# Kernel optimization log

Measured on AMD Instinct MI355X. Metric: run time of the kernel, lower is better.

The kernel has to match this reference:

```python
import jax, jax.numpy as jnp
import numpy as np

N = 50000
E = 800000
EPS = 1e-16
NEG_SLOPE = 0.2

def setup_inputs() -> dict:
    key = jax.random.key(0)
    ks = jax.random.split(key, 10)
    s = lambda fan: 1.0 / np.sqrt(fan)
    return {
        "x": jax.random.normal(ks[0], (N, 128), dtype=jnp.float32),
        "edge_index": jax.random.randint(ks[1], (2, E), 0, N, dtype=jnp.int64),
        "W1": jax.random.normal(ks[2], (128, 4 * 32), dtype=jnp.float32) * s(128),
        "att_src1": jax.random.normal(ks[3], (4, 32), dtype=jnp.float32) * s(32),
        "att_dst1": jax.random.normal(ks[4], (4, 32), dtype=jnp.float32) * s(32),
        "b1": jnp.zeros((128,), dtype=jnp.float32),
        "W2": jax.random.normal(ks[5], (128, 2), dtype=jnp.float32) * s(128),
        "att_src2": jax.random.normal(ks[6], (1, 2), dtype=jnp.float32) * s(2),
        "att_dst2": jax.random.normal(ks[7], (1, 2), dtype=jnp.float32) * s(2),
        "b2": jnp.zeros((2,), dtype=jnp.float32),
    }

def _gat_conv(x, src, dst, W, att_src, att_dst, bias, heads, out_ch, concat):
    n = x.shape[0]
    h = (x @ W).reshape(n, heads, out_ch)                      # [N,H,C]
    a_src = jnp.sum(h * att_src[None], axis=-1)                # [N,H]
    a_dst = jnp.sum(h * att_dst[None], axis=-1)                # [N,H]
    e = jax.nn.leaky_relu(a_src[src] + a_dst[dst], NEG_SLOPE)  # [Etot,H]
    # segment softmax over incoming edges per destination node
    m = jax.ops.segment_max(e, dst, num_segments=n)            # [N,H]
    m = jnp.where(jnp.isfinite(m), m, 0.0)
    ex = jnp.exp(e - m[dst])
    denom = jax.ops.segment_sum(ex, dst, num_segments=n)       # [N,H]
    alpha = ex / (denom[dst] + EPS)                            # [Etot,H]
    out = jax.ops.segment_sum(alpha[:, :, None] * h[src], dst, num_segments=n)  # [N,H,C]
    if concat:
        out = out.reshape(n, heads * out_ch)
    else:
        out = out.mean(axis=1)
    return out + bias

def reference(x, edge_index, W1, att_src1, att_dst1, b1, W2, att_src2, att_dst2, b2):
    n = x.shape[0]
    # PyG GATConv adds self-loops by default
    loops = jnp.arange(n, dtype=edge_index.dtype)
    src = jnp.concatenate([edge_index[0], loops])
    dst = jnp.concatenate([edge_index[1], loops])
    # dropout is identity at inference
    h = jax.nn.elu(_gat_conv(x, src, dst, W1, att_src1, att_dst1, b1, 4, 32, True))
    h = _gat_conv(h, src, dst, W2, att_src2, att_dst2, b2, 1, 2, False)
    return jax.nn.log_softmax(h, axis=1)
```

## Files before the change

kernel.cpp:

```cpp
#include <hip/hip_runtime.h>
#include <hip/hip_bf16.h>

#define NN 50000
#define EE 800000
#define ET (EE + NN)
#define CAP 64
#define NEG_SLOPE 0.2f
#define EPSF 1e-16f
#define BUILD_BLOCKS 4096
#define GEMM_BLOCKS ((NN + 63) / 64)

typedef unsigned int uint32;
typedef __attribute__((ext_vector_type(8))) short short8;
typedef __attribute__((ext_vector_type(4))) float floatx4;

__device__ __forceinline__ unsigned short f2bf(float f) {
  unsigned int u = __float_as_uint(f);
  unsigned int r = (u + 0x7fffu + ((u >> 16) & 1u)) >> 16;
  return (unsigned short)r;
}
__device__ __forceinline__ float bf_lo(uint32 v) { return __uint_as_float(v << 16); }
__device__ __forceinline__ float bf_hi(uint32 v) { return __uint_as_float(v & 0xffff0000u); }


__device__ __forceinline__ void do_build(int b, int nb, const int* __restrict__ ei,
                                         int* __restrict__ counts,
                                         int* __restrict__ csr) {
  const int range = b & 7;
  const int lo = range * (NN / 8);
  const int hi = lo + (NN / 8);
  const int group = b >> 3;
  const int ngr = nb >> 3;
  for (int i = group * 256 + threadIdx.x; i < ET; i += ngr * 256) {
    int d = (i < EE) ? ei[EE + i] : (i - EE);
    if (d >= lo && d < hi) {
      int s = (i < EE) ? ei[i] : d;
      int r = atomicAdd(&counts[d], 1);
      if (r < CAP) csr[d * CAP + r] = s;
    }
  }
}

__device__ __forceinline__ void do_gemm_tile(
    int tile, const float* __restrict__ x, const unsigned short* __restrict__ Wt,
    const float* __restrict__ att_src1, const float* __restrict__ att_dst1,
    uint32* __restrict__ h1b, float* __restrict__ as1, float* __restrict__ ad1) {
  const int t    = threadIdx.x;
  const int wave = t >> 6;
  const int lane = t & 63;
  const int quad = lane >> 4;
  const int col  = lane & 15;
  const int nodeBase = tile * 64 + wave * 16;

  floatx4 acc[8];
  #pragma unroll
  for (int i = 0; i < 8; i++) acc[i] = (floatx4){0.f, 0.f, 0.f, 0.f};

  int mread = nodeBase + col; if (mread >= NN) mread = NN - 1;
  const float* __restrict__ xrow = x + (size_t)mread * 128 + quad * 8;
  const unsigned short* __restrict__ bbase = Wt + col * 128 + quad * 8;

  #pragma unroll
  for (int ks = 0; ks < 4; ks++) {
    float4 a0 = *(const float4*)(xrow + ks * 32);
    float4 a1 = *(const float4*)(xrow + ks * 32 + 4);
    union { short8 v; unsigned short u[8]; } af;
    af.u[0] = f2bf(a0.x); af.u[1] = f2bf(a0.y);
    af.u[2] = f2bf(a0.z); af.u[3] = f2bf(a0.w);
    af.u[4] = f2bf(a1.x); af.u[5] = f2bf(a1.y);
    af.u[6] = f2bf(a1.z); af.u[7] = f2bf(a1.w);
    #pragma unroll
    for (int tt = 0; tt < 8; tt++) {
      short8 bf = *(const short8*)(bbase + tt * 16 * 128 + ks * 32);
      acc[tt] = __builtin_amdgcn_mfma_f32_16x16x32_bf16(af.v, bf, acc[tt], 0, 0, 0);
    }
  }

  float asv[8], adv[8];
  #pragma unroll
  for (int tt = 0; tt < 8; tt++) {
    asv[tt] = att_src1[tt * 16 + col];
    adv[tt] = att_dst1[tt * 16 + col];
  }

  #pragma unroll
  for (int r = 0; r < 4; r++) {
    const int gn = nodeBase + quad * 4 + r;
    const bool live = (gn < NN);
    #pragma unroll
    for (int tt = 0; tt < 8; tt++) {
      float v = acc[tt][r];
      float w = __shfl_xor(v, 1, 64);
      if (live && ((col & 1) == 0)) {
        uint32 pk = (uint32)f2bf(v) | ((uint32)f2bf(w) << 16);
        h1b[(size_t)gn * 64 + tt * 8 + (col >> 1)] = pk;
      }
    }
    #pragma unroll
    for (int h = 0; h < 4; h++) {
      float ps = acc[2 * h][r] * asv[2 * h] + acc[2 * h + 1][r] * asv[2 * h + 1];
      float pd = acc[2 * h][r] * adv[2 * h] + acc[2 * h + 1][r] * adv[2 * h + 1];
      #pragma unroll
      for (int off = 1; off < 16; off <<= 1) {
        ps += __shfl_xor(ps, off, 64);
        pd += __shfl_xor(pd, off, 64);
      }
      if (live && col == 0) {
        as1[gn * 4 + h] = ps;
        ad1[gn * 4 + h] = pd;
      }
    }
  }
}

__device__ __forceinline__ void do_agg1_group(
    int g, const int* __restrict__ counts, const int* __restrict__ csr,
    const uint32* __restrict__ h1b, const float* __restrict__ as1,
    const float* __restrict__ ad1, const float* __restrict__ b1,
    const float* __restrict__ W2, const float* __restrict__ att_src2,
    const float* __restrict__ att_dst2,
    float* __restrict__ h2, float* __restrict__ as2, float* __restrict__ ad2) {
  const int lane = threadIdx.x & 63;
  const int wv = threadIdx.x >> 6;
  const int hd = lane >> 4;
  const int n = __builtin_amdgcn_readfirstlane(g * 4 + wv);

  const int cnt = __builtin_amdgcn_readfirstlane(counts[n]);
  const int* __restrict__ row = csr + n * CAP;
  const float adv = ad1[n * 4 + hd];

  float den = 0.f, accx = 0.f, accy = 0.f;
  int j = 0;
  for (; j + 3 < cnt; j += 4) {
    int s0 = row[j], s1 = row[j + 1], s2 = row[j + 2], s3 = row[j + 3];
    float e0 = as1[s0 * 4 + hd] + adv;
    float e1 = as1[s1 * 4 + hd] + adv;
    float e2 = as1[s2 * 4 + hd] + adv;
    float e3 = as1[s3 * 4 + hd] + adv;
    uint32 v0 = h1b[s0 * 64 + lane];
    uint32 v1 = h1b[s1 * 64 + lane];
    uint32 v2 = h1b[s2 * 64 + lane];
    uint32 v3 = h1b[s3 * 64 + lane];
    e0 = (e0 > 0.f) ? e0 : NEG_SLOPE * e0;
    e1 = (e1 > 0.f) ? e1 : NEG_SLOPE * e1;
    e2 = (e2 > 0.f) ? e2 : NEG_SLOPE * e2;
    e3 = (e3 > 0.f) ? e3 : NEG_SLOPE * e3;
    float x0 = __expf(e0), x1 = __expf(e1), x2 = __expf(e2), x3 = __expf(e3);
    den += (x0 + x1) + (x2 + x3);
    accx = fmaf(x0, bf_lo(v0), accx);
    accy = fmaf(x0, bf_hi(v0), accy);
    accx = fmaf(x1, bf_lo(v1), accx);
    accy = fmaf(x1, bf_hi(v1), accy);
    accx = fmaf(x2, bf_lo(v2), accx);
    accy = fmaf(x2, bf_hi(v2), accy);
    accx = fmaf(x3, bf_lo(v3), accx);
    accy = fmaf(x3, bf_hi(v3), accy);
  }
  for (; j < cnt; j++) {
    int s = row[j];
    float e = as1[s * 4 + hd] + adv;
    e = (e > 0.f) ? e : NEG_SLOPE * e;
    float ex = __expf(e);
    uint32 v = h1b[s * 64 + lane];
    den += ex;
    accx = fmaf(ex, bf_lo(v), accx);
    accy = fmaf(ex, bf_hi(v), accy);
  }

  float inv = 1.f / (den + EPSF);
  float2 bb = ((const float2*)b1)[lane];
  float ox = accx * inv + bb.x;
  float oy = accy * inv + bb.y;
  ox = (ox > 0.f) ? ox : (__expf(ox) - 1.f);
  oy = (oy > 0.f) ? oy : (__expf(oy) - 1.f);

  float4 wq = ((const float4*)W2)[lane];
  float p0 = ox * wq.x + oy * wq.z;
  float p1 = ox * wq.y + oy * wq.w;
  #pragma unroll
  for (int off = 32; off; off >>= 1) {
    p0 += __shfl_xor(p0, off, 64);
    p1 += __shfl_xor(p1, off, 64);
  }
  if (lane == 0) {
    *(float2*)&h2[n * 2] = make_float2(p0, p1);
    as2[n] = p0 * att_src2[0] + p1 * att_src2[1];
    ad2[n] = p0 * att_dst2[0] + p1 * att_dst2[1];
  }
}

__device__ __forceinline__ void do_agg2_item(
    int i, const int* __restrict__ counts, const int* __restrict__ csr,
    const float* __restrict__ h2, const float* __restrict__ as2,
    const float* __restrict__ ad2, const float* __restrict__ b2,
    float* __restrict__ out) {
  int n = i >> 3;
  int sub = i & 7;
  const float adv = ad2[n];
  const int cnt = counts[n];
  const int* __restrict__ row = csr + n * CAP;
  const float2* __restrict__ h2v = (const float2*)h2;

  float den = 0.f, a0 = 0.f, a1 = 0.f;
  for (int j = sub; j < cnt; j += 8) {
    int s = row[j];
    float e = as2[s] + adv;
    e = (e > 0.f) ? e : NEG_SLOPE * e;
    float ex = __expf(e);
    float2 hv = h2v[s];
    den += ex;
    a0 = fmaf(ex, hv.x, a0);
    a1 = fmaf(ex, hv.y, a1);
  }
  #pragma unroll
  for (int off = 4; off; off >>= 1) {
    den += __shfl_down(den, off, 8);
    a0  += __shfl_down(a0, off, 8);
    a1  += __shfl_down(a1, off, 8);
  }
  if (sub == 0) {
    float inv = 1.f / (den + EPSF);
    float o0 = a0 * inv + b2[0];
    float o1 = a1 * inv + b2[1];
    float mx = fmaxf(o0, o1);
    float lse = mx + __logf(__expf(o0 - mx) + __expf(o1 - mx));
    *(float2*)&out[n * 2] = make_float2(o0 - lse, o1 - lse);
  }
}

__global__ __launch_bounds__(256) void prep_zero_k(
    const float* __restrict__ W1, unsigned short* __restrict__ Wt,
    int* __restrict__ counts) {
  const int step = gridDim.x * 256;
  for (int i = blockIdx.x * 256 + threadIdx.x; i < NN; i += step) counts[i] = 0;
  for (int i = blockIdx.x * 256 + threadIdx.x; i < 128 * 128; i += step) {
    int k = i >> 7, c = i & 127;
    Wt[c * 128 + k] = f2bf(W1[i]);
  }
}

__global__ __launch_bounds__(256) void work_k(
    const int* __restrict__ ei, int* __restrict__ counts, int* __restrict__ csr,
    const float* __restrict__ x, const unsigned short* __restrict__ Wt,
    const float* __restrict__ att_src1, const float* __restrict__ att_dst1,
    uint32* __restrict__ h1b, float* __restrict__ as1, float* __restrict__ ad1) {
  const int b = blockIdx.x;
  if (b < BUILD_BLOCKS) {
    do_build(b, BUILD_BLOCKS, ei, counts, csr);
  } else {
    do_gemm_tile(b - BUILD_BLOCKS, x, Wt, att_src1, att_dst1, h1b, as1, ad1);
  }
}

__global__ __launch_bounds__(256) void agg1_k(
    const int* __restrict__ counts, const int* __restrict__ csr,
    const uint32* __restrict__ h1b, const float* __restrict__ as1,
    const float* __restrict__ ad1, const float* __restrict__ b1,
    const float* __restrict__ W2, const float* __restrict__ att_src2,
    const float* __restrict__ att_dst2,
    float* __restrict__ h2, float* __restrict__ as2, float* __restrict__ ad2) {
  do_agg1_group(blockIdx.x, counts, csr, h1b, as1, ad1, b1, W2,
                att_src2, att_dst2, h2, as2, ad2);
}

__global__ __launch_bounds__(256) void agg2_k(
    const int* __restrict__ counts, const int* __restrict__ csr,
    const float* __restrict__ h2, const float* __restrict__ as2,
    const float* __restrict__ ad2, const float* __restrict__ b2,
    float* __restrict__ out) {
  int i = blockIdx.x * 256 + threadIdx.x;
  if (i < NN * 8) do_agg2_item(i, counts, csr, h2, as2, ad2, b2, out);
}

extern "C" void kernel_launch(void* const* d_in, const int* in_sizes, int n_in,
                              void* d_out, int out_size, void* d_ws, size_t ws_size,
                              hipStream_t stream) {
  const float* x        = (const float*)d_in[0];
  const int*   ei       = (const int*)d_in[1];
  const float* W1       = (const float*)d_in[2];
  const float* att_src1 = (const float*)d_in[3];
  const float* att_dst1 = (const float*)d_in[4];
  const float* b1       = (const float*)d_in[5];
  const float* W2       = (const float*)d_in[6];
  const float* att_src2 = (const float*)d_in[7];
  const float* att_dst2 = (const float*)d_in[8];
  const float* b2       = (const float*)d_in[9];
  float* out = (float*)d_out;

  char* p = (char*)d_ws;
  auto alloc = [&](size_t bytes) {
    char* r = p;
    p += (bytes + 255) & ~size_t(255);
    return r;
  };
  uint32* h1b  = (uint32*)alloc(sizeof(uint32) * NN * 64);
  float* as1   = (float*)alloc(sizeof(float) * NN * 4);
  float* ad1   = (float*)alloc(sizeof(float) * NN * 4);
  float* h2    = (float*)alloc(sizeof(float) * NN * 2);
  float* as2   = (float*)alloc(sizeof(float) * NN);
  float* ad2   = (float*)alloc(sizeof(float) * NN);
  int*   counts = (int*)alloc(sizeof(int) * NN);
  int*   csr   = (int*)alloc(sizeof(int) * NN * CAP);
  unsigned short* Wt = (unsigned short*)alloc(sizeof(unsigned short) * 128 * 128);

  prep_zero_k<<<256, 256, 0, stream>>>(W1, Wt, counts);
  work_k<<<BUILD_BLOCKS + GEMM_BLOCKS, 256, 0, stream>>>(
      ei, counts, csr, x, Wt, att_src1, att_dst1, h1b, as1, ad1);
  agg1_k<<<NN / 4, 256, 0, stream>>>(counts, csr, h1b, as1, ad1, b1, W2,
                                     att_src2, att_dst2, h2, as2, ad2);
  agg2_k<<<(NN * 8 + 255) / 256, 256, 0, stream>>>(counts, csr, h2, as2, ad2,
                                                   b2, out);
}
```

Measured before the change: 195.8 us.

## Store CSR as 16-bit indices, vectorize edge loads, handle self-loops inline

CSR neighbor indices are now stored as 16-bit values, which fit because the node count is below 65536. This halves the scattered CSR write and read traffic. The build loop reads edge endpoints as int4 vectors and no longer inserts self-loops into the CSR. Instead, both aggregation kernels add the self-loop term directly from the node's own features, and agg1 fetches four neighbor indices with a single 8-byte load. This relies on the node count staying under 65536, and the self-loop no longer uses up a slot in the capped rows.

```diff
diff --git a/kernel.cpp b/kernel.cpp
--- a/kernel.cpp
+++ b/kernel.cpp
@@ -3,7 +3,6 @@
 
 #define NN 50000
 #define EE 800000
-#define ET (EE + NN)
 #define CAP 64
 #define NEG_SLOPE 0.2f
 #define EPSF 1e-16f
@@ -11,6 +10,7 @@
 #define GEMM_BLOCKS ((NN + 63) / 64)
 
 typedef unsigned int uint32;
+typedef unsigned short ushort16;
 typedef __attribute__((ext_vector_type(8))) short short8;
 typedef __attribute__((ext_vector_type(4))) float floatx4;
 
@@ -21,22 +21,36 @@
 }
 __device__ __forceinline__ float bf_lo(uint32 v) { return __uint_as_float(v << 16); }
 __device__ __forceinline__ float bf_hi(uint32 v) { return __uint_as_float(v & 0xffff0000u); }
-
+__device__ __forceinline__ float lrelu(float e) { return (e > 0.f) ? e : NEG_SLOPE * e; }
 
 __device__ __forceinline__ void do_build(int b, int nb, const int* __restrict__ ei,
                                          int* __restrict__ counts,
-                                         int* __restrict__ csr) {
+                                         ushort16* __restrict__ csr) {
   const int range = b & 7;
   const int lo = range * (NN / 8);
   const int hi = lo + (NN / 8);
   const int group = b >> 3;
   const int ngr = nb >> 3;
-  for (int i = group * 256 + threadIdx.x; i < ET; i += ngr * 256) {
-    int d = (i < EE) ? ei[EE + i] : (i - EE);
-    if (d >= lo && d < hi) {
-      int s = (i < EE) ? ei[i] : d;
-      int r = atomicAdd(&counts[d], 1);
-      if (r < CAP) csr[d * CAP + r] = s;
+  const int4* __restrict__ dst4 = (const int4*)(ei + EE);
+  const int4* __restrict__ src4 = (const int4*)ei;
+  for (int c = group * 256 + threadIdx.x; c < EE / 4; c += ngr * 256) {
+    int4 d = dst4[c];
+    int4 s = src4[c];
+    if (d.x >= lo && d.x < hi) {
+      int r = atomicAdd(&counts[d.x], 1);
+      if (r < CAP) csr[d.x * CAP + r] = (ushort16)s.x;
+    }
+    if (d.y >= lo && d.y < hi) {
+      int r = atomicAdd(&counts[d.y], 1);
+      if (r < CAP) csr[d.y * CAP + r] = (ushort16)s.y;
+    }
+    if (d.z >= lo && d.z < hi) {
+      int r = atomicAdd(&counts[d.z], 1);
+      if (r < CAP) csr[d.z * CAP + r] = (ushort16)s.z;
+    }
+    if (d.w >= lo && d.w < hi) {
+      int r = atomicAdd(&counts[d.w], 1);
+      if (r < CAP) csr[d.w * CAP + r] = (ushort16)s.w;
     }
   }
 }
@@ -113,26 +127,56 @@
   }
 }
 
-__device__ __forceinline__ void do_agg1_group(
-    int g, const int* __restrict__ counts, const int* __restrict__ csr,
+__global__ __launch_bounds__(256) void prep_zero_k(
+    const float* __restrict__ W1, unsigned short* __restrict__ Wt,
+    int* __restrict__ counts) {
+  const int step = gridDim.x * 256;
+  for (int i = blockIdx.x * 256 + threadIdx.x; i < NN; i += step) counts[i] = 0;
+  for (int i = blockIdx.x * 256 + threadIdx.x; i < 128 * 128; i += step) {
+    int k = i >> 7, c = i & 127;
+    Wt[c * 128 + k] = f2bf(W1[i]);
+  }
+}
+
+__global__ __launch_bounds__(256) void work_k(
+    const int* __restrict__ ei, int* __restrict__ counts, ushort16* __restrict__ csr,
+    const float* __restrict__ x, const unsigned short* __restrict__ Wt,
+    const float* __restrict__ att_src1, const float* __restrict__ att_dst1,
+    uint32* __restrict__ h1b, float* __restrict__ as1, float* __restrict__ ad1) {
+  const int b = blockIdx.x;
+  if (b < BUILD_BLOCKS) {
+    do_build(b, BUILD_BLOCKS, ei, counts, csr);
+  } else {
+    do_gemm_tile(b - BUILD_BLOCKS, x, Wt, att_src1, att_dst1, h1b, as1, ad1);
+  }
+}
+
+__global__ __launch_bounds__(256) void agg1_k(
+    const int* __restrict__ counts, const ushort16* __restrict__ csr,
     const uint32* __restrict__ h1b, const float* __restrict__ as1,
     const float* __restrict__ ad1, const float* __restrict__ b1,
     const float* __restrict__ W2, const float* __restrict__ att_src2,
     const float* __restrict__ att_dst2,
     float* __restrict__ h2, float* __restrict__ as2, float* __restrict__ ad2) {
   const int lane = threadIdx.x & 63;
-  const int wv = threadIdx.x >> 6;
+  const int n = __builtin_amdgcn_readfirstlane(blockIdx.x * 4 + (threadIdx.x >> 6));
   const int hd = lane >> 4;
-  const int n = __builtin_amdgcn_readfirstlane(g * 4 + wv);
 
   const int cnt = __builtin_amdgcn_readfirstlane(counts[n]);
-  const int* __restrict__ row = csr + n * CAP;
+  const ushort16* __restrict__ row = csr + n * CAP;
   const float adv = ad1[n * 4 + hd];
 
-  float den = 0.f, accx = 0.f, accy = 0.f;
+  float es = lrelu(as1[n * 4 + hd] + adv);
+  float xs = __expf(es);
+  uint32 vs = h1b[n * 64 + lane];
+  float den = xs;
+  float accx = xs * bf_lo(vs), accy = xs * bf_hi(vs);
+
   int j = 0;
   for (; j + 3 < cnt; j += 4) {
-    int s0 = row[j], s1 = row[j + 1], s2 = row[j + 2], s3 = row[j + 3];
+    union { uint2 v; ushort16 u[4]; } ss;
+    ss.v = *(const uint2*)(row + j);
+    int s0 = ss.u[0], s1 = ss.u[1], s2 = ss.u[2], s3 = ss.u[3];
     float e0 = as1[s0 * 4 + hd] + adv;
     float e1 = as1[s1 * 4 + hd] + adv;
     float e2 = as1[s2 * 4 + hd] + adv;
@@ -141,11 +185,8 @@
     uint32 v1 = h1b[s1 * 64 + lane];
     uint32 v2 = h1b[s2 * 64 + lane];
     uint32 v3 = h1b[s3 * 64 + lane];
-    e0 = (e0 > 0.f) ? e0 : NEG_SLOPE * e0;
-    e1 = (e1 > 0.f) ? e1 : NEG_SLOPE * e1;
-    e2 = (e2 > 0.f) ? e2 : NEG_SLOPE * e2;
-    e3 = (e3 > 0.f) ? e3 : NEG_SLOPE * e3;
-    float x0 = __expf(e0), x1 = __expf(e1), x2 = __expf(e2), x3 = __expf(e3);
+    float x0 = __expf(lrelu(e0)), x1 = __expf(lrelu(e1));
+    float x2 = __expf(lrelu(e2)), x3 = __expf(lrelu(e3));
     den += (x0 + x1) + (x2 + x3);
     accx = fmaf(x0, bf_lo(v0), accx);
     accy = fmaf(x0, bf_hi(v0), accy);
@@ -158,8 +199,7 @@
   }
   for (; j < cnt; j++) {
     int s = row[j];
-    float e = as1[s * 4 + hd] + adv;
-    e = (e > 0.f) ? e : NEG_SLOPE * e;
+    float e = lrelu(as1[s * 4 + hd] + adv);
     float ex = __expf(e);
     uint32 v = h1b[s * 64 + lane];
     den += ex;
@@ -189,24 +229,29 @@
   }
 }
 
-__device__ __forceinline__ void do_agg2_item(
-    int i, const int* __restrict__ counts, const int* __restrict__ csr,
+__global__ __launch_bounds__(256) void agg2_k(
+    const int* __restrict__ counts, const ushort16* __restrict__ csr,
     const float* __restrict__ h2, const float* __restrict__ as2,
     const float* __restrict__ ad2, const float* __restrict__ b2,
     float* __restrict__ out) {
+  int i = blockIdx.x * 256 + threadIdx.x;
+  if (i >= NN * 8) return;
   int n = i >> 3;
   int sub = i & 7;
   const float adv = ad2[n];
   const int cnt = counts[n];
-  const int* __restrict__ row = csr + n * CAP;
+  const ushort16* __restrict__ row = csr + n * CAP;
   const float2* __restrict__ h2v = (const float2*)h2;
 
   float den = 0.f, a0 = 0.f, a1 = 0.f;
+  if (sub == 0) {
+    float xs = __expf(lrelu(as2[n] + adv));
+    float2 hv = h2v[n];
+    den = xs; a0 = xs * hv.x; a1 = xs * hv.y;
+  }
   for (int j = sub; j < cnt; j += 8) {
     int s = row[j];
-    float e = as2[s] + adv;
-    e = (e > 0.f) ? e : NEG_SLOPE * e;
-    float ex = __expf(e);
+    float ex = __expf(lrelu(as2[s] + adv));
     float2 hv = h2v[s];
     den += ex;
     a0 = fmaf(ex, hv.x, a0);
@@ -226,50 +271,6 @@
     float lse = mx + __logf(__expf(o0 - mx) + __expf(o1 - mx));
     *(float2*)&out[n * 2] = make_float2(o0 - lse, o1 - lse);
   }
-}
-
-__global__ __launch_bounds__(256) void prep_zero_k(
-    const float* __restrict__ W1, unsigned short* __restrict__ Wt,
-    int* __restrict__ counts) {
-  const int step = gridDim.x * 256;
-  for (int i = blockIdx.x * 256 + threadIdx.x; i < NN; i += step) counts[i] = 0;
-  for (int i = blockIdx.x * 256 + threadIdx.x; i < 128 * 128; i += step) {
-    int k = i >> 7, c = i & 127;
-    Wt[c * 128 + k] = f2bf(W1[i]);
-  }
-}
-
-__global__ __launch_bounds__(256) void work_k(
-    const int* __restrict__ ei, int* __restrict__ counts, int* __restrict__ csr,
-    const float* __restrict__ x, const unsigned short* __restrict__ Wt,
-    const float* __restrict__ att_src1, const float* __restrict__ att_dst1,
-    uint32* __restrict__ h1b, float* __restrict__ as1, float* __restrict__ ad1) {
-  const int b = blockIdx.x;
-  if (b < BUILD_BLOCKS) {
-    do_build(b, BUILD_BLOCKS, ei, counts, csr);
-  } else {
-    do_gemm_tile(b - BUILD_BLOCKS, x, Wt, att_src1, att_dst1, h1b, as1, ad1);
-  }
-}
-
-__global__ __launch_bounds__(256) void agg1_k(
-    const int* __restrict__ counts, const int* __restrict__ csr,
-    const uint32* __restrict__ h1b, const float* __restrict__ as1,
-    const float* __restrict__ ad1, const float* __restrict__ b1,
-    const float* __restrict__ W2, const float* __restrict__ att_src2,
-    const float* __restrict__ att_dst2,
-    float* __restrict__ h2, float* __restrict__ as2, float* __restrict__ ad2) {
-  do_agg1_group(blockIdx.x, counts, csr, h1b, as1, ad1, b1, W2,
-                att_src2, att_dst2, h2, as2, ad2);
-}
-
-__global__ __launch_bounds__(256) void agg2_k(
-    const int* __restrict__ counts, const int* __restrict__ csr,
-    const float* __restrict__ h2, const float* __restrict__ as2,
-    const float* __restrict__ ad2, const float* __restrict__ b2,
-    float* __restrict__ out) {
-  int i = blockIdx.x * 256 + threadIdx.x;
-  if (i < NN * 8) do_agg2_item(i, counts, csr, h2, as2, ad2, b2, out);
 }
 
 extern "C" void kernel_launch(void* const* d_in, const int* in_sizes, int n_in,
@@ -300,7 +301,7 @@
   float* as2   = (float*)alloc(sizeof(float) * NN);
   float* ad2   = (float*)alloc(sizeof(float) * NN);
   int*   counts = (int*)alloc(sizeof(int) * NN);
-  int*   csr   = (int*)alloc(sizeof(int) * NN * CAP);
+  ushort16* csr = (ushort16*)alloc(sizeof(ushort16) * NN * CAP);
   unsigned short* Wt = (unsigned short*)alloc(sizeof(unsigned short) * 128 * 128);
 
   prep_zero_k<<<256, 256, 0, stream>>>(W1, Wt, counts);
```

New measurement: 196.1 us. Within noise of the previous version (+0.1%).
